# Kernel tuning notes

Measured on AMD Instinct MI355X. Metric: run time of the kernel, lower is better.

## Reference

```python
import jax, jax.numpy as jnp
import numpy as np

B, L, DM, H = 64, 512, 1024, 1024


def setup_inputs() -> dict:
    key = jax.random.key(0)
    ks = jax.random.split(key, 6)
    graph_feature = jax.random.normal(ks[0], (DM,), dtype=jnp.float32)
    x_tensors = jax.random.normal(ks[1], (B, 3, L, DM), dtype=jnp.float32)
    # per-(batch, level) valid lengths in [1, L]; mask True == padding
    lengths = jax.random.randint(ks[2], (B, 3), 1, L + 1)
    mask = jnp.arange(L)[None, None, :] >= lengths[..., None]  # [B,3,L] bool
    W_proj = jax.random.normal(ks[3], (H, DM), dtype=jnp.float32) / np.float32(np.sqrt(DM))
    b_proj = jnp.zeros((H,), dtype=jnp.float32)
    W_comb = jax.random.normal(ks[4], (3, DM), dtype=jnp.float32) / np.float32(np.sqrt(DM))
    b_comb = jnp.zeros((3,), dtype=jnp.float32)
    return {"graph_feature": graph_feature, "x_tensors": x_tensors, "mask": mask,
            "W_proj": W_proj, "b_proj": b_proj, "W_comb": W_comb, "b_comb": b_comb}


def reference(graph_feature, x_tensors, mask, W_proj, b_proj, W_comb, b_comb):
    # projector: Linear(mm_hidden -> hidden) over all tokens of all 3 levels
    proj = jnp.einsum('bkld,hd->bklh', x_tensors, W_proj) + b_proj  # [B,3,L,H]
    # combiner weights over (node, motif, graph); graph_feature is [DM]
    weights = jax.nn.softmax(W_comb @ graph_feature + b_comb)  # [3]
    node_w, motif_w, graph_w = weights[0], weights[1], weights[2]
    # masked mean pooling per (batch, level); mask True == padding
    valid = (~mask).astype(proj.dtype)  # [B,3,L]
    sums = jnp.einsum('bklh,bkl->bkh', proj, valid)  # [B,3,H]
    counts = valid.sum(axis=-1)[..., None]  # [B,3,1]
    pooled = sums / counts  # [B,3,H]; level 0=node, 1=motif, 2=graph
    node_p, motif_p, graph_p = pooled[:, 0], pooled[:, 1], pooled[:, 2]
    feature = graph_w * graph_p + motif_w * motif_p + node_w * node_p  # [B,H]
    return feature
```

## Files before the change

kernel.cpp:

```cpp
#include <hip/hip_runtime.h>

#define DM   1024
#define LSEQ 512
#define NBK  192
#define NCH  8
#define HDIM 1024

__global__ __launch_bounds__(256) void detect_kernel(
    const unsigned* __restrict__ m, int* __restrict__ flag)
{
    __shared__ int s[256];
    const int t = threadIdx.x;
    unsigned any = 0;
    for (int i = t; i < (NBK * LSEQ / 4); i += 256)
        any |= m[i] & 0xFFFFFF00u;
    s[t] = (any != 0);
    __syncthreads();
    for (int sf = 128; sf > 0; sf >>= 1) {
        if (t < sf) s[t] |= s[t + sf];
        __syncthreads();
    }
    if (t == 0) *flag = (s[0] == 0) ? 1 : 0;
}

__global__ __launch_bounds__(256) void prep_kernel(
    const float* __restrict__ gf, const unsigned char* __restrict__ mask,
    const float* __restrict__ Wc, const float* __restrict__ bc,
    const int* __restrict__ flagp,
    float* __restrict__ w, int* __restrict__ cnts, float* __restrict__ y)
{
    const int bid = blockIdx.x, t = threadIdx.x;
    y[bid * 256 + t] = 0.0f;

    if (bid < NBK) {
        __shared__ int sc[256];
        int c = 0;
        if (*flagp) {
            const unsigned* row = (const unsigned*)mask + bid * LSEQ;
            c = (int)(row[t] == 0) + (int)(row[t + 256] == 0);
        } else {
            if (t < 128) {
                unsigned u = ((const unsigned*)mask)[bid * 128 + t];
                c = (int)((u & 0xFFu) == 0) + (int)((u & 0xFF00u) == 0)
                  + (int)((u & 0xFF0000u) == 0) + (int)((u & 0xFF000000u) == 0);
            }
        }
        sc[t] = c;
        __syncthreads();
        for (int s = 128; s > 0; s >>= 1) {
            if (t < s) sc[t] += sc[t + s];
            __syncthreads();
        }
        if (t == 0) cnts[bid] = sc[0];
    } else if (bid == NBK) {
        __shared__ float sz0[256], sz1[256], sz2[256];
        float p0 = 0.f, p1 = 0.f, p2 = 0.f;
        #pragma unroll
        for (int j = 0; j < 4; ++j) {
            float g = gf[t * 4 + j];
            p0 += Wc[0 * DM + t * 4 + j] * g;
            p1 += Wc[1 * DM + t * 4 + j] * g;
            p2 += Wc[2 * DM + t * 4 + j] * g;
        }
        sz0[t] = p0; sz1[t] = p1; sz2[t] = p2;
        __syncthreads();
        for (int s = 128; s > 0; s >>= 1) {
            if (t < s) { sz0[t] += sz0[t+s]; sz1[t] += sz1[t+s]; sz2[t] += sz2[t+s]; }
            __syncthreads();
        }
        if (t == 0) {
            float z0 = sz0[0] + bc[0], z1 = sz1[0] + bc[1], z2 = sz2[0] + bc[2];
            float m  = fmaxf(z0, fmaxf(z1, z2));
            float e0 = expf(z0 - m), e1 = expf(z1 - m), e2 = expf(z2 - m);
            float inv = 1.0f / (e0 + e1 + e2);
            w[0] = e0 * inv; w[1] = e1 * inv; w[2] = e2 * inv;
        }
    }
}

__global__ __launch_bounds__(256) void pool_kernel(
    const float4* __restrict__ x4, const float* __restrict__ w,
    const int* __restrict__ cnts, float* __restrict__ y)
{
    const int bid = blockIdx.x;
    const int bk  = bid >> 3;
    const int ch  = bid & 7;
    const int len = cnts[bk];
    const int l0  = ch << 6;
    if (l0 >= len) return;
    const int nrows = min(64, len - l0);

    const int t = threadIdx.x;
    const int b = bk / 3;
    const int k = bk - b * 3;
    const float scale = w[k] / (float)len;

    const float4* xp = x4 + ((bk * LSEQ + l0) * (DM / 4)) + t;

    float ax0=0.f, ay0=0.f, az0=0.f, aw0=0.f;
    float ax1=0.f, ay1=0.f, az1=0.f, aw1=0.f;
    int r = 0;
    for (; r + 2 <= nrows; r += 2) {
        float4 v0 = xp[(r    ) * (DM / 4)];
        float4 v1 = xp[(r + 1) * (DM / 4)];
        ax0 += v0.x; ay0 += v0.y; az0 += v0.z; aw0 += v0.w;
        ax1 += v1.x; ay1 += v1.y; az1 += v1.z; aw1 += v1.w;
    }
    if (r < nrows) {
        float4 v0 = xp[r * (DM / 4)];
        ax0 += v0.x; ay0 += v0.y; az0 += v0.z; aw0 += v0.w;
    }
    ax0 = (ax0 + ax1) * scale;
    ay0 = (ay0 + ay1) * scale;
    az0 = (az0 + az1) * scale;
    aw0 = (aw0 + aw1) * scale;

    float* yp = y + b * DM + t * 4;
    atomicAdd(yp + 0, ax0);
    atomicAdd(yp + 1, ay0);
    atomicAdd(yp + 2, az0);
    atomicAdd(yp + 3, aw0);
}

__global__ __launch_bounds__(256) void out_kernel(
    const float4* __restrict__ y4, const float4* __restrict__ W4,
    const float4* __restrict__ bp4, float4* __restrict__ out4)
{
    __shared__ float ylds[64 * 129];
    const int t  = threadIdx.x;
    const int b  = t & 63;
    const int hh = t >> 6;
    const int h  = (blockIdx.x << 2) + hh;

    float acc = 0.f;
    for (int c = 0; c < 8; ++c) {
        __syncthreads();
        #pragma unroll
        for (int j = 0; j < 8; ++j) {
            int flat = j * 256 + t;
            int row  = flat >> 5;
            int col4 = flat & 31;
            float4 v = y4[row * 256 + c * 32 + col4];
            float* p = &ylds[row * 129 + (col4 << 2)];
            p[0] = v.x; p[1] = v.y; p[2] = v.z; p[3] = v.w;
        }
        __syncthreads();
        const float* yr = &ylds[b * 129];
        #pragma unroll
        for (int j = 0; j < 32; ++j) {
            float4 wv = W4[h * 256 + c * 32 + j];
            int i = j << 2;
            acc += yr[i]     * wv.x + yr[i + 1] * wv.y
                 + yr[i + 2] * wv.z + yr[i + 3] * wv.w;
        }
    }

    __syncthreads();
    ylds[hh * 64 + b] = acc;
    __syncthreads();
    if (t < 64) {
        float4 bv = bp4[blockIdx.x];
        float4 v;
        v.x = ylds[0 * 64 + t] + bv.x;
        v.y = ylds[1 * 64 + t] + bv.y;
        v.z = ylds[2 * 64 + t] + bv.z;
        v.w = ylds[3 * 64 + t] + bv.w;
        out4[t * (HDIM / 4) + blockIdx.x] = v;
    }
}

extern "C" void kernel_launch(void* const* d_in, const int* in_sizes, int n_in,
                              void* d_out, int out_size, void* d_ws, size_t ws_size,
                              hipStream_t stream) {
    const float*         gf   = (const float*)d_in[0];
    const float*         x    = (const float*)d_in[1];
    const unsigned char* mask = (const unsigned char*)d_in[2];
    const float*         Wp   = (const float*)d_in[3];
    const float*         bp   = (const float*)d_in[4];
    const float*         Wc   = (const float*)d_in[5];
    const float*         bc   = (const float*)d_in[6];
    float* out = (float*)d_out;

    float* wsf  = (float*)d_ws;
    float* w    = wsf;
    int*   cnts = (int*)(wsf + 4);
    int*   flag = (int*)(wsf + 196);
    float* y    = wsf + 256;

    detect_kernel<<<1, 256, 0, stream>>>((const unsigned*)mask, flag);
    prep_kernel<<<256, 256, 0, stream>>>(gf, mask, Wc, bc, flag, w, cnts, y);
    pool_kernel<<<NBK * NCH, 256, 0, stream>>>((const float4*)x, w, cnts, y);
    out_kernel<<<HDIM / 4, 256, 0, stream>>>((const float4*)y, (const float4*)Wp,
                                             (const float4*)bp, (float4*)out);
}
```

Measured before the change: 568.7 us.

## Replace atomic pooling with partial-sum buffer and separate reduce kernel

Pooling blocks now write per-chunk partial sums to a workspace buffer instead of atomically adding into y, and a new reduce kernel applies the combiner weights and 1/len scaling. The mask counting moves into the pool kernel itself, and the flag detection and softmax weights are merged into one two-block kernel, removing the separate prep launch and the zeroing of y. This trades atomic contention and one kernel launch for an extra kernel and an extra round trip through a partial buffer of up to about 6 MB.

```diff
diff --git a/kernel.cpp b/kernel.cpp
--- a/kernel.cpp
+++ b/kernel.cpp
@@ -6,53 +6,28 @@
 #define NCH  8
 #define HDIM 1024
 
-__global__ __launch_bounds__(256) void detect_kernel(
-    const unsigned* __restrict__ m, int* __restrict__ flag)
-{
-    __shared__ int s[256];
+#define PART_OFF 256
+#define Y_OFF    (256 + 1536 * 1024)
+
+__global__ __launch_bounds__(256) void detectw_kernel(
+    const unsigned* __restrict__ m, const float* __restrict__ gf,
+    const float* __restrict__ Wc, const float* __restrict__ bc,
+    int* __restrict__ flag, float* __restrict__ w)
+{
     const int t = threadIdx.x;
-    unsigned any = 0;
-    for (int i = t; i < (NBK * LSEQ / 4); i += 256)
-        any |= m[i] & 0xFFFFFF00u;
-    s[t] = (any != 0);
-    __syncthreads();
-    for (int sf = 128; sf > 0; sf >>= 1) {
-        if (t < sf) s[t] |= s[t + sf];
-        __syncthreads();
-    }
-    if (t == 0) *flag = (s[0] == 0) ? 1 : 0;
-}
-
-__global__ __launch_bounds__(256) void prep_kernel(
-    const float* __restrict__ gf, const unsigned char* __restrict__ mask,
-    const float* __restrict__ Wc, const float* __restrict__ bc,
-    const int* __restrict__ flagp,
-    float* __restrict__ w, int* __restrict__ cnts, float* __restrict__ y)
-{
-    const int bid = blockIdx.x, t = threadIdx.x;
-    y[bid * 256 + t] = 0.0f;
-
-    if (bid < NBK) {
-        __shared__ int sc[256];
-        int c = 0;
-        if (*flagp) {
-            const unsigned* row = (const unsigned*)mask + bid * LSEQ;
-            c = (int)(row[t] == 0) + (int)(row[t + 256] == 0);
-        } else {
-            if (t < 128) {
-                unsigned u = ((const unsigned*)mask)[bid * 128 + t];
-                c = (int)((u & 0xFFu) == 0) + (int)((u & 0xFF00u) == 0)
-                  + (int)((u & 0xFF0000u) == 0) + (int)((u & 0xFF000000u) == 0);
-            }
-        }
-        sc[t] = c;
-        __syncthreads();
-        for (int s = 128; s > 0; s >>= 1) {
-            if (t < s) sc[t] += sc[t + s];
+    if (blockIdx.x == 0) {
+        __shared__ int s[256];
+        unsigned any = 0;
+        for (int i = t; i < (NBK * LSEQ / 4); i += 256)
+            any |= m[i] & 0xFFFFFF00u;
+        s[t] = (any != 0);
+        __syncthreads();
+        for (int sf = 128; sf > 0; sf >>= 1) {
+            if (t < sf) s[t] |= s[t + sf];
             __syncthreads();
         }
-        if (t == 0) cnts[bid] = sc[0];
-    } else if (bid == NBK) {
+        if (t == 0) *flag = (s[0] == 0) ? 1 : 0;
+    } else {
         __shared__ float sz0[256], sz1[256], sz2[256];
         float p0 = 0.f, p1 = 0.f, p2 = 0.f;
         #pragma unroll
@@ -70,30 +45,48 @@
         }
         if (t == 0) {
             float z0 = sz0[0] + bc[0], z1 = sz1[0] + bc[1], z2 = sz2[0] + bc[2];
-            float m  = fmaxf(z0, fmaxf(z1, z2));
-            float e0 = expf(z0 - m), e1 = expf(z1 - m), e2 = expf(z2 - m);
+            float mx = fmaxf(z0, fmaxf(z1, z2));
+            float e0 = expf(z0 - mx), e1 = expf(z1 - mx), e2 = expf(z2 - mx);
             float inv = 1.0f / (e0 + e1 + e2);
             w[0] = e0 * inv; w[1] = e1 * inv; w[2] = e2 * inv;
         }
     }
 }
 
-__global__ __launch_bounds__(256) void pool_kernel(
-    const float4* __restrict__ x4, const float* __restrict__ w,
-    const int* __restrict__ cnts, float* __restrict__ y)
-{
+__global__ __launch_bounds__(256) void pool2_kernel(
+    const float4* __restrict__ x4, const unsigned char* __restrict__ mask,
+    const int* __restrict__ flagp, float4* __restrict__ part,
+    int* __restrict__ cnts)
+{
+    __shared__ int sc[256];
     const int bid = blockIdx.x;
     const int bk  = bid >> 3;
     const int ch  = bid & 7;
-    const int len = cnts[bk];
-    const int l0  = ch << 6;
+    const int t   = threadIdx.x;
+
+    int c = 0;
+    if (*flagp) {
+        const unsigned* row = (const unsigned*)mask + bk * LSEQ;
+        c = (int)(row[t] == 0) + (int)(row[t + 256] == 0);
+    } else {
+        if (t < 128) {
+            unsigned u = ((const unsigned*)mask)[bk * 128 + t];
+            c = (int)((u & 0xFFu) == 0) + (int)((u & 0xFF00u) == 0)
+              + (int)((u & 0xFF0000u) == 0) + (int)((u & 0xFF000000u) == 0);
+        }
+    }
+    sc[t] = c;
+    __syncthreads();
+    for (int s = 128; s > 0; s >>= 1) {
+        if (t < s) sc[t] += sc[t + s];
+        __syncthreads();
+    }
+    const int len = sc[0];
+    if (ch == 0 && t == 0) cnts[bk] = len;
+
+    const int l0 = ch << 6;
     if (l0 >= len) return;
     const int nrows = min(64, len - l0);
-
-    const int t = threadIdx.x;
-    const int b = bk / 3;
-    const int k = bk - b * 3;
-    const float scale = w[k] / (float)len;
 
     const float4* xp = x4 + ((bk * LSEQ + l0) * (DM / 4)) + t;
 
@@ -110,16 +103,32 @@
         float4 v0 = xp[r * (DM / 4)];
         ax0 += v0.x; ay0 += v0.y; az0 += v0.z; aw0 += v0.w;
     }
-    ax0 = (ax0 + ax1) * scale;
-    ay0 = (ay0 + ay1) * scale;
-    az0 = (az0 + az1) * scale;
-    aw0 = (aw0 + aw1) * scale;
-
-    float* yp = y + b * DM + t * 4;
-    atomicAdd(yp + 0, ax0);
-    atomicAdd(yp + 1, ay0);
-    atomicAdd(yp + 2, az0);
-    atomicAdd(yp + 3, aw0);
+    float4 v;
+    v.x = ax0 + ax1; v.y = ay0 + ay1; v.z = az0 + az1; v.w = aw0 + aw1;
+    part[bid * 256 + t] = v;
+}
+
+__global__ __launch_bounds__(256) void reduce_kernel(
+    const float4* __restrict__ part, const float* __restrict__ w,
+    const int* __restrict__ cnts, float4* __restrict__ y4)
+{
+    const int b = blockIdx.x;
+    const int t = threadIdx.x;
+    float4 acc; acc.x = acc.y = acc.z = acc.w = 0.f;
+    #pragma unroll
+    for (int k = 0; k < 3; ++k) {
+        const int bk  = b * 3 + k;
+        const int len = cnts[bk];
+        const int nch = (len + 63) >> 6;
+        const float s = w[k] / (float)len;
+        const float4* p = part + bk * 8 * 256 + t;
+        for (int chv = 0; chv < nch; ++chv) {
+            float4 v = p[chv * 256];
+            acc.x += s * v.x; acc.y += s * v.y;
+            acc.z += s * v.z; acc.w += s * v.w;
+        }
+    }
+    y4[b * 256 + t] = acc;
 }
 
 __global__ __launch_bounds__(256) void out_kernel(
@@ -181,15 +190,19 @@
     const float*         bc   = (const float*)d_in[6];
     float* out = (float*)d_out;
 
-    float* wsf  = (float*)d_ws;
-    float* w    = wsf;
-    int*   cnts = (int*)(wsf + 4);
-    int*   flag = (int*)(wsf + 196);
-    float* y    = wsf + 256;
-
-    detect_kernel<<<1, 256, 0, stream>>>((const unsigned*)mask, flag);
-    prep_kernel<<<256, 256, 0, stream>>>(gf, mask, Wc, bc, flag, w, cnts, y);
-    pool_kernel<<<NBK * NCH, 256, 0, stream>>>((const float4*)x, w, cnts, y);
+    float*  wsf  = (float*)d_ws;
+    float*  w    = wsf;
+    int*    cnts = (int*)(wsf + 4);
+    int*    flag = (int*)(wsf + 196);
+    float4* part = (float4*)(wsf + PART_OFF);
+    float*  y    = wsf + Y_OFF;
+
+    detectw_kernel<<<2, 256, 0, stream>>>((const unsigned*)mask, gf, Wc, bc,
+                                          flag, w);
+    pool2_kernel<<<NBK * NCH, 256, 0, stream>>>((const float4*)x, mask, flag,
+                                                part, cnts);
+    reduce_kernel<<<64, 256, 0, stream>>>((const float4*)part, w, cnts,
+                                          (float4*)y);
     out_kernel<<<HDIM / 4, 256, 0, stream>>>((const float4*)y, (const float4*)Wp,
                                              (const float4*)bp, (float4*)out);
 }
```

Result: no change. 575.1 us (+1.1%).
